# Kernel tuning notes

Hardware: AMD Instinct MI355X
Metric: run time of the kernel (lower is better)

## Reference

```python
import jax, jax.numpy as jnp
import numpy as np


def setup_inputs() -> dict:
    key = jax.random.key(0)
    k1, k2 = jax.random.split(key)
    B, S, L, E = 8, 256, 64, 128
    note_embedding = jax.random.normal(k1, (B, S, E), dtype=jnp.float32)
    harmony_embedding = jax.random.normal(k2, (B, L, E), dtype=jnp.float32)
    return {"note_embedding": note_embedding, "harmony_embedding": harmony_embedding}


def reference(note_embedding, harmony_embedding):
    # note_embedding: [B, S, E], harmony_embedding: [B, L, E]
    B, S, E = note_embedding.shape
    scale = 1.0 / jnp.sqrt(jnp.asarray(E, dtype=note_embedding.dtype))
    # raw[b,l,t] = harmony[b,l] . note[b,t]; the per-segment score is
    # sum_t softmax_t(raw*scale over [start,end]) * raw[b,l,t], since
    # (harmony * (attn @ values)).sum(-1) == attn @ (harmony . note_t).
    raw = jnp.einsum('ble,bse->bls', harmony_embedding, note_embedding)  # [B,L,S]
    logits = raw * scale
    pos = jnp.arange(S)

    def per_start(start):
        mask = pos >= start                                # [S]
        z = jnp.where(mask, logits, -jnp.inf)              # [B,L,S]
        m = jnp.max(z, axis=-1, keepdims=True)             # suffix max (finite)
        ez = jnp.exp(z - m)                                # 0 where masked
        c1 = jnp.cumsum(ez, axis=-1)                       # running softmax denom
        c2 = jnp.cumsum(ez * raw, axis=-1)                 # running weighted sum
        denom = jnp.where(c1 == 0, 1.0, c1)
        return jnp.where(mask, c2 / denom, 0.0)            # [B,L,S] indexed by end

    # [S_start, B, L, S_end] -> [B, S_start, S_end, L]; zeros where end < start
    scores = jax.vmap(per_start)(pos)
    return jnp.transpose(scores, (1, 0, 3, 2))
```

## Files before the change

### kernel.cpp

```cpp
#include <hip/hip_runtime.h>
#include <hip/hip_bf16.h>

#define B_ 8
#define S_ 256
#define L_ 64
#define E_ 128

__global__ __launch_bounds__(64) void prep_kernel(const float* __restrict__ note,
                                                  const float* __restrict__ harmony,
                                                  float2* __restrict__ ws) {
    const int b = blockIdx.x / L_;
    const int l = blockIdx.x % L_;
    const int lane = threadIdx.x;

    __shared__ float h[E_];
    const float* hp = harmony + (size_t)(b * L_ + l) * E_;
    h[lane]      = hp[lane];
    h[lane + 64] = hp[lane + 64];
    __syncthreads();

    float raw[4];
#pragma unroll
    for (int k = 0; k < 4; ++k) {
        const int s = lane + 64 * k;
        const float4* nv = reinterpret_cast<const float4*>(note + (size_t)(b * S_ + s) * E_);
        float acc = 0.f;
#pragma unroll
        for (int e = 0; e < E_ / 4; ++e) {
            float4 v = nv[e];
            acc += h[4 * e + 0] * v.x + h[4 * e + 1] * v.y +
                   h[4 * e + 2] * v.z + h[4 * e + 3] * v.w;
        }
        raw[k] = acc;
    }

    const float scale = 0.088388347648318447f;

    float m = fmaxf(fmaxf(raw[0], raw[1]), fmaxf(raw[2], raw[3]));
#pragma unroll
    for (int off = 1; off < 64; off <<= 1)
        m = fmaxf(m, __shfl_xor(m, off, 64));
    m *= scale;

#pragma unroll
    for (int k = 0; k < 4; ++k) {
        const int s = lane + 64 * k;
        float e_ = __expf(raw[k] * scale - m);
        ws[(size_t)(b * S_ + s) * L_ + l] = make_float2(e_, e_ * raw[k]);
    }
}

__global__ __launch_bounds__(64) void score_kernel(const float2* __restrict__ ws,
                                                   float* __restrict__ out) {
    const int b     = blockIdx.x >> 8;
    const int start = blockIdx.x & 255;
    const int l     = threadIdx.x;

    float* orow = out + ((size_t)(b * S_ + start) * S_) * L_ + l;

    for (int end = 0; end < start; ++end)
        orow[(size_t)end * L_] = 0.f;

    const float2* w = ws + (size_t)(b * S_) * L_ + l;
    float c1 = 0.f, c2 = 0.f;
#pragma unroll 4
    for (int end = start; end < S_; ++end) {
        float2 v = w[(size_t)end * L_];
        c1 += v.x;
        c2 += v.y;
        orow[(size_t)end * L_] = c2 * __builtin_amdgcn_rcpf(c1);
    }
}

extern "C" void kernel_launch(void* const* d_in, const int* in_sizes, int n_in,
                              void* d_out, int out_size, void* d_ws, size_t ws_size,
                              hipStream_t stream) {
    const float* note    = (const float*)d_in[0];
    const float* harmony = (const float*)d_in[1];
    float2* ws           = (float2*)d_ws;
    float* out           = (float*)d_out;

    hipLaunchKernelGGL(prep_kernel, dim3(B_ * L_), dim3(64), 0, stream,
                       note, harmony, ws);
    hipLaunchKernelGGL(score_kernel, dim3(B_ * S_), dim3(64), 0, stream,
                       ws, out);
}
```

Before: 157.2 us.

## Precompute prefix sums in prep and compute scores as prefix differences

The prep kernel now builds inclusive prefix sums of the exp weights and weighted raw values along the sequence with a wave-level scan. The score kernel then computes each output as a difference of two prefix entries, which removes the serial per-start cumulative loop. This lets the score work be spread over many 256-thread blocks that each handle a 64-end chunk and write vectorised float4 stores. The cost is possible cancellation error when subtracting large prefix sums, and more global reads of P per output.

```diff
diff --git a/kernel.cpp b/kernel.cpp
--- a/kernel.cpp
+++ b/kernel.cpp
@@ -8,7 +8,7 @@
 
 __global__ __launch_bounds__(64) void prep_kernel(const float* __restrict__ note,
                                                   const float* __restrict__ harmony,
-                                                  float2* __restrict__ ws) {
+                                                  float2* __restrict__ P) {
     const int b = blockIdx.x / L_;
     const int l = blockIdx.x % L_;
     const int lane = threadIdx.x;
@@ -22,7 +22,7 @@
     float raw[4];
 #pragma unroll
     for (int k = 0; k < 4; ++k) {
-        const int s = lane + 64 * k;
+        const int s = 64 * k + lane;
         const float4* nv = reinterpret_cast<const float4*>(note + (size_t)(b * S_ + s) * E_);
         float acc = 0.f;
 #pragma unroll
@@ -42,33 +42,70 @@
         m = fmaxf(m, __shfl_xor(m, off, 64));
     m *= scale;
 
+    float carry1 = 0.f, carry2 = 0.f;
 #pragma unroll
     for (int k = 0; k < 4; ++k) {
-        const int s = lane + 64 * k;
-        float e_ = __expf(raw[k] * scale - m);
-        ws[(size_t)(b * S_ + s) * L_ + l] = make_float2(e_, e_ * raw[k]);
+        float x1 = __expf(raw[k] * scale - m);
+        float x2 = x1 * raw[k];
+#pragma unroll
+        for (int off = 1; off < 64; off <<= 1) {
+            float y1 = __shfl_up(x1, off, 64);
+            float y2 = __shfl_up(x2, off, 64);
+            if (lane >= off) { x1 += y1; x2 += y2; }
+        }
+        const int s = 64 * k + lane;
+        P[(size_t)(b * S_ + s) * L_ + l] = make_float2(carry1 + x1, carry2 + x2);
+        carry1 += __shfl(x1, 63, 64);
+        carry2 += __shfl(x2, 63, 64);
     }
 }
 
-__global__ __launch_bounds__(64) void score_kernel(const float2* __restrict__ ws,
-                                                   float* __restrict__ out) {
-    const int b     = blockIdx.x >> 8;
-    const int start = blockIdx.x & 255;
-    const int l     = threadIdx.x;
+__global__ __launch_bounds__(256) void score_kernel(const float* __restrict__ P,
+                                                    float* __restrict__ out) {
+    const int bid   = blockIdx.x;
+    const int c     = bid & 3;
+    const int start = (bid >> 2) & 255;
+    const int b     = bid >> 10;
 
-    float* orow = out + ((size_t)(b * S_ + start) * S_) * L_ + l;
+    const int lg   = threadIdx.x & 15;
+    const int esub = threadIdx.x >> 4;
+    const int l4   = lg * 4;
+    const int end0 = c * 64;
 
-    for (int end = 0; end < start; ++end)
-        orow[(size_t)end * L_] = 0.f;
+    float* obase = out + ((size_t)(b * S_ + start)) * S_ * L_;
 
-    const float2* w = ws + (size_t)(b * S_) * L_ + l;
-    float c1 = 0.f, c2 = 0.f;
-#pragma unroll 4
-    for (int end = start; end < S_; ++end) {
-        float2 v = w[(size_t)end * L_];
-        c1 += v.x;
-        c2 += v.y;
-        orow[(size_t)end * L_] = c2 * __builtin_amdgcn_rcpf(c1);
+    if (end0 + 63 < start) {
+        const float4 z = make_float4(0.f, 0.f, 0.f, 0.f);
+#pragma unroll
+        for (int j = 0; j < 4; ++j) {
+            const int end = end0 + j * 16 + esub;
+            *reinterpret_cast<float4*>(obase + (size_t)end * L_ + l4) = z;
+        }
+        return;
+    }
+
+    float4 qa, qb;
+    if (start > 0) {
+        const float* qrow = P + ((size_t)(b * S_ + start - 1)) * L_ * 2;
+        qa = *reinterpret_cast<const float4*>(qrow + l4 * 2);
+        qb = *reinterpret_cast<const float4*>(qrow + l4 * 2 + 4);
+    } else {
+        qa = qb = make_float4(0.f, 0.f, 0.f, 0.f);
+    }
+
+#pragma unroll
+    for (int j = 0; j < 4; ++j) {
+        const int end = end0 + j * 16 + esub;
+        const float* prow = P + ((size_t)(b * S_ + end)) * L_ * 2;
+        float4 pa = *reinterpret_cast<const float4*>(prow + l4 * 2);
+        float4 pb = *reinterpret_cast<const float4*>(prow + l4 * 2 + 4);
+        const bool ok = (end >= start);
+        float4 r;
+        r.x = ok ? (pa.y - qa.y) / (pa.x - qa.x) : 0.f;
+        r.y = ok ? (pa.w - qa.w) / (pa.z - qa.z) : 0.f;
+        r.z = ok ? (pb.y - qb.y) / (pb.x - qb.x) : 0.f;
+        r.w = ok ? (pb.w - qb.w) / (pb.z - qb.z) : 0.f;
+        *reinterpret_cast<float4*>(obase + (size_t)end * L_ + l4) = r;
     }
 }
 
@@ -77,11 +114,11 @@
                               hipStream_t stream) {
     const float* note    = (const float*)d_in[0];
     const float* harmony = (const float*)d_in[1];
-    float2* ws           = (float2*)d_ws;
+    float2* P            = (float2*)d_ws;
     float* out           = (float*)d_out;
 
     hipLaunchKernelGGL(prep_kernel, dim3(B_ * L_), dim3(64), 0, stream,
-                       note, harmony, ws);
-    hipLaunchKernelGGL(score_kernel, dim3(B_ * S_), dim3(64), 0, stream,
-                       ws, out);
+                       note, harmony, P);
+    hipLaunchKernelGGL(score_kernel, dim3(B_ * S_ * (S_ / 64)), dim3(256), 0, stream,
+                       (const float*)P, out);
 }
```

Measured after the change: 157.2 us. About the same (+0.0%).
